# Optimization experiments

Measured on AMD Instinct MI355X. Metric: run time of the kernel, lower is better.

Reference implementation:

```python
import jax, jax.numpy as jnp
import numpy as np

N = 100000   # num variables
D_IN = 512
D_OUT = 512
C = 4096     # num clusters
K = 32       # vars per cluster
E = 16384    # cluster edges
S = 16       # shared vars per edge
H = 4        # num heads
NEG_SLOPE = 0.2


def setup_inputs() -> dict:
    key = jax.random.key(0)
    ks = jax.random.split(key, 8)
    xav = (6.0 / (D_IN + D_OUT)) ** 0.5  # xavier_uniform bound
    x_var = jax.random.normal(ks[0], (N, D_IN), dtype=jnp.float32)
    W_Q = jax.random.uniform(ks[1], (D_OUT, D_IN), jnp.float32, -xav, xav)
    W_K = jax.random.uniform(ks[2], (D_OUT, D_IN), jnp.float32, -xav, xav)
    W_V = jax.random.uniform(ks[3], (D_OUT, D_IN), jnp.float32, -xav, xav)
    head_weights = jnp.ones((H,), jnp.float32)
    cluster_var_ids = jax.random.randint(ks[4], (C, K), 0, N)
    cluster_edge_index = jax.random.randint(ks[5], (2, E), 0, C)
    shared_vars = jax.random.randint(ks[6], (E, S), 0, N)
    return {
        'x_var': x_var, 'W_Q': W_Q, 'W_K': W_K, 'W_V': W_V,
        'head_weights': head_weights,
        'cluster_var_ids': cluster_var_ids,
        'cluster_edge_index': cluster_edge_index,
        'shared_vars': shared_vars,
        'active_heads': 4,
    }


def reference(x_var, W_Q, W_K, W_V, head_weights,
              cluster_var_ids, cluster_edge_index, shared_vars, active_heads):
    # Per-cluster mean pooling over member variables: [C, D_in]
    cluster_feats = x_var[cluster_var_ids].mean(axis=1)
    # Linear projections (torch Linear: y = x @ W.T)
    Q = cluster_feats @ W_Q.T   # [C, D_out]
    Kc = cluster_feats @ W_K.T  # [C, D_out]
    V = cluster_feats @ W_V.T   # [C, D_out]
    c1 = cluster_edge_index[0]  # [E] source clusters
    c2 = cluster_edge_index[1]  # [E] target clusters
    # Scalar dot-product attention per cluster edge
    scale = jnp.asarray(D_OUT, jnp.float32) ** 0.5
    scores = jnp.einsum('ed,ed->e', Q[c1], Kc[c2]) / scale
    scores = jnp.where(scores >= 0, scores, NEG_SLOPE * scores)  # leaky_relu
    attn = jax.nn.sigmoid(scores) * head_weights[:active_heads].mean()  # [E]
    # Per-edge message = attn * V[c2], broadcast to each shared var of the edge
    upd = attn[:, None] * V[c2]                                   # [E, D_out]
    upd_flat = jnp.broadcast_to(upd[:, None, :], (E, S, D_OUT)).reshape(E * S, D_OUT)
    x_out = x_var.at[shared_vars.reshape(-1)].add(upd_flat)
    return x_out
```

## Files before the change

kernel.cpp:

```cpp
#include <hip/hip_runtime.h>
#include <hip/hip_bf16.h>
#include <math.h>

#define N_VARS    100000
#define D_DIM     512
#define C_CLUST   4096
#define K_VARS    32
#define E_EDGES   16384
#define S_SHARED  16
#define H_HEADS   4
#define CAP       32
#define NEG_SLOPE 0.2f

typedef __bf16 bf16x8_t __attribute__((ext_vector_type(8)));
typedef float  f32x4_t  __attribute__((ext_vector_type(4)));

__device__ __forceinline__ unsigned int f32_to_bf16_bits(float f) {
    unsigned int u = __builtin_bit_cast(unsigned int, f);
    unsigned int lsb = (u >> 16) & 1u;
    u += 0x7fffu + lsb;
    return u >> 16;
}
__device__ __forceinline__ unsigned int pack_bf16x2(float a, float b) {
    return (f32_to_bf16_bits(b) << 16) | f32_to_bf16_bits(a);
}
__device__ __forceinline__ float bf16_lo_to_f32(unsigned int w) {
    return __builtin_bit_cast(float, w << 16);
}
__device__ __forceinline__ float bf16_hi_to_f32(unsigned int w) {
    return __builtin_bit_cast(float, w & 0xffff0000u);
}

__device__ __forceinline__ int decode_active_heads(const int* p) {
    int raw = p[0];
    if (raw >= 1 && raw <= H_HEADS) return raw;
    float f = __builtin_bit_cast(float, raw);
    if (f >= 1.0f && f <= (float)H_HEADS) return (int)f;
    return H_HEADS;
}

__global__ void convert_w_kernel(const float* __restrict__ Wq,
                                 const float* __restrict__ Wk,
                                 const float* __restrict__ Wv,
                                 unsigned int* __restrict__ Wb) {
    const float* W = (blockIdx.y == 0) ? Wq : (blockIdx.y == 1) ? Wk : Wv;
    int i = blockIdx.x * blockDim.x + threadIdx.x;
    float2 w = ((const float2*)W)[i];
    Wb[(size_t)blockIdx.y * (D_DIM * D_DIM / 2) + i] = pack_bf16x2(w.x, w.y);
}

__global__ void pool_kernel(const float* __restrict__ x,
                            const int* __restrict__ cvid,
                            uint2* __restrict__ cfb ,
                            int* __restrict__ counts) {
    int gtid = blockIdx.x * blockDim.x + threadIdx.x;
    if (gtid < N_VARS) counts[gtid] = 0;

    int c = blockIdx.x * 2 + (threadIdx.x >> 7);
    c = __builtin_amdgcn_readfirstlane(c);
    int t = threadIdx.x & 127;
    const int* cv = cvid + c * K_VARS;
    float4 acc = {0.f, 0.f, 0.f, 0.f};
#pragma unroll 8
    for (int k = 0; k < K_VARS; ++k) {
        int v = cv[k];
        float4 w = ((const float4*)(x + (size_t)v * D_DIM))[t];
        acc.x += w.x; acc.y += w.y; acc.z += w.z; acc.w += w.w;
    }
    const float inv = 1.0f / (float)K_VARS;
    uint2 o;
    o.x = pack_bf16x2(acc.x * inv, acc.y * inv);
    o.y = pack_bf16x2(acc.z * inv, acc.w * inv);
    cfb[(size_t)c * (D_DIM / 4) + t] = o;
}

__global__ __launch_bounds__(256) void gemm_kernel(
        const unsigned short* __restrict__ cfb,
        const unsigned short* __restrict__ Wb,
        float* __restrict__ Qo, float* __restrict__ Ko,
        unsigned short* __restrict__ Vb) {
    const unsigned short* W = Wb + (size_t)blockIdx.z * D_DIM * D_DIM;

    int wave = threadIdx.x >> 6;
    int lane = threadIdx.x & 63;
    int m0 = blockIdx.x * 64 + wave * 16;
    int n0 = blockIdx.y * 64;
    int mr = m0 + (lane & 15);
    int kb = (lane >> 4) * 8;

    f32x4_t acc0 = {0.f,0.f,0.f,0.f}, acc1 = {0.f,0.f,0.f,0.f};
    f32x4_t acc2 = {0.f,0.f,0.f,0.f}, acc3 = {0.f,0.f,0.f,0.f};
    const unsigned short* arow = cfb + (size_t)mr * D_DIM + kb;
    const unsigned short* b0r  = W + (size_t)(n0 +  0 + (lane & 15)) * D_DIM + kb;
    const unsigned short* b1r  = W + (size_t)(n0 + 16 + (lane & 15)) * D_DIM + kb;
    const unsigned short* b2r  = W + (size_t)(n0 + 32 + (lane & 15)) * D_DIM + kb;
    const unsigned short* b3r  = W + (size_t)(n0 + 48 + (lane & 15)) * D_DIM + kb;
#pragma unroll 4
    for (int k0 = 0; k0 < D_DIM; k0 += 32) {
        bf16x8_t a  = *(const bf16x8_t*)(arow + k0);
        bf16x8_t b0 = *(const bf16x8_t*)(b0r + k0);
        bf16x8_t b1 = *(const bf16x8_t*)(b1r + k0);
        bf16x8_t b2 = *(const bf16x8_t*)(b2r + k0);
        bf16x8_t b3 = *(const bf16x8_t*)(b3r + k0);
        acc0 = __builtin_amdgcn_mfma_f32_16x16x32_bf16(a, b0, acc0, 0, 0, 0);
        acc1 = __builtin_amdgcn_mfma_f32_16x16x32_bf16(a, b1, acc1, 0, 0, 0);
        acc2 = __builtin_amdgcn_mfma_f32_16x16x32_bf16(a, b2, acc2, 0, 0, 0);
        acc3 = __builtin_amdgcn_mfma_f32_16x16x32_bf16(a, b3, acc3, 0, 0, 0);
    }
    int rb = m0 + (lane >> 4) * 4;
    int cl = lane & 15;
    if (blockIdx.z < 2) {
        float* O = (blockIdx.z == 0) ? Qo : Ko;
#pragma unroll
        for (int r = 0; r < 4; ++r) {
            float* orow = O + (size_t)(rb + r) * D_DIM + n0 + cl;
            orow[ 0] = acc0[r];
            orow[16] = acc1[r];
            orow[32] = acc2[r];
            orow[48] = acc3[r];
        }
    } else {
#pragma unroll
        for (int r = 0; r < 4; ++r) {
            unsigned short* orow = Vb + (size_t)(rb + r) * D_DIM + n0 + cl;
            orow[ 0] = (unsigned short)f32_to_bf16_bits(acc0[r]);
            orow[16] = (unsigned short)f32_to_bf16_bits(acc1[r]);
            orow[32] = (unsigned short)f32_to_bf16_bits(acc2[r]);
            orow[48] = (unsigned short)f32_to_bf16_bits(acc3[r]);
        }
    }
}

__global__ __launch_bounds__(256) void score_fill_kernel(
        const float* __restrict__ Q,
        const float* __restrict__ Kc,
        const int* __restrict__ cei,
        const float* __restrict__ hw,
        const int* __restrict__ active_heads,
        const int* __restrict__ shared_vars,
        int* __restrict__ counts,
        unsigned int* __restrict__ bucket) {
    int e = __builtin_amdgcn_readfirstlane(blockIdx.x * 4 + (threadIdx.x >> 6));
    int lane = threadIdx.x & 63;
    int c1 = cei[e];
    int c2 = cei[E_EDGES + e];
    const float4* q = (const float4*)(Q  + (size_t)c1 * D_DIM);
    const float4* k = (const float4*)(Kc + (size_t)c2 * D_DIM);
    float4 qa = q[lane], qb = q[lane + 64];
    float4 ka = k[lane], kb = k[lane + 64];
    float s = qa.x*ka.x + qa.y*ka.y + qa.z*ka.z + qa.w*ka.w
            + qb.x*kb.x + qb.y*kb.y + qb.z*kb.z + qb.w*kb.w;
#pragma unroll
    for (int off = 32; off > 0; off >>= 1)
        s += __shfl_xor(s, off);
    int ah = decode_active_heads(active_heads);
    float m = 0.f;
    for (int h = 0; h < ah; ++h) m += hw[h];
    m /= (float)ah;
    float sc = s * (1.0f / sqrtf((float)D_DIM));
    sc = sc >= 0.f ? sc : NEG_SLOPE * sc;
    float attn = m / (1.f + __expf(-sc));
    unsigned int packed = (f32_to_bf16_bits(attn) << 16) | (unsigned int)c2;
    if (lane < S_SHARED) {
        int v = shared_vars[e * S_SHARED + lane];
        int pos = atomicAdd(&counts[v], 1);
        if (pos < CAP) bucket[(size_t)v * CAP + pos] = packed;
    }
}

__global__ __launch_bounds__(256) void gather_kernel(
        const float* __restrict__ x,
        const unsigned short* __restrict__ V,
        const int* __restrict__ counts,
        const unsigned int* __restrict__ bucket,
        float* __restrict__ out) {
    int v = __builtin_amdgcn_readfirstlane(blockIdx.x * 4 + (threadIdx.x >> 6));
    int lane = threadIdx.x & 63;
    const f32x4_t* xr = (const f32x4_t*)(x + (size_t)v * D_DIM);
    f32x4_t a0 = xr[2 * lane];
    f32x4_t a1 = xr[2 * lane + 1];
    int cnt = counts[v];
    if (cnt > CAP) cnt = CAP;
    const unsigned int* bk = bucket + (size_t)v * CAP;
    uint4 pw = *(const uint4*)bk;

    int k = 0;
    while (k < cnt) {
        int m = cnt - k;
        uint4 w0, w1, w2, w3;
        w0 = ((const uint4*)(V + (size_t)(pw.x & 0xFFFu) * D_DIM))[lane];
        if (m > 1) w1 = ((const uint4*)(V + (size_t)(pw.y & 0xFFFu) * D_DIM))[lane];
        if (m > 2) w2 = ((const uint4*)(V + (size_t)(pw.z & 0xFFFu) * D_DIM))[lane];
        if (m > 3) w3 = ((const uint4*)(V + (size_t)(pw.w & 0xFFFu) * D_DIM))[lane];
        uint4 pwn;
        int kn = k + 4;
        if (kn < cnt) pwn = *(const uint4*)(bk + kn);

        float t0 = bf16_hi_to_f32(pw.x >> 16 << 16);
        {
            float at = __builtin_bit_cast(float, pw.x & 0xffff0000u);
            a0[0] += at * bf16_lo_to_f32(w0.x); a0[1] += at * bf16_hi_to_f32(w0.x);
            a0[2] += at * bf16_lo_to_f32(w0.y); a0[3] += at * bf16_hi_to_f32(w0.y);
            a1[0] += at * bf16_lo_to_f32(w0.z); a1[1] += at * bf16_hi_to_f32(w0.z);
            a1[2] += at * bf16_lo_to_f32(w0.w); a1[3] += at * bf16_hi_to_f32(w0.w);
        }
        if (m > 1) {
            float at = __builtin_bit_cast(float, pw.y & 0xffff0000u);
            a0[0] += at * bf16_lo_to_f32(w1.x); a0[1] += at * bf16_hi_to_f32(w1.x);
            a0[2] += at * bf16_lo_to_f32(w1.y); a0[3] += at * bf16_hi_to_f32(w1.y);
            a1[0] += at * bf16_lo_to_f32(w1.z); a1[1] += at * bf16_hi_to_f32(w1.z);
            a1[2] += at * bf16_lo_to_f32(w1.w); a1[3] += at * bf16_hi_to_f32(w1.w);
        }
        if (m > 2) {
            float at = __builtin_bit_cast(float, pw.z & 0xffff0000u);
            a0[0] += at * bf16_lo_to_f32(w2.x); a0[1] += at * bf16_hi_to_f32(w2.x);
            a0[2] += at * bf16_lo_to_f32(w2.y); a0[3] += at * bf16_hi_to_f32(w2.y);
            a1[0] += at * bf16_lo_to_f32(w2.z); a1[1] += at * bf16_hi_to_f32(w2.z);
            a1[2] += at * bf16_lo_to_f32(w2.w); a1[3] += at * bf16_hi_to_f32(w2.w);
        }
        if (m > 3) {
            float at = __builtin_bit_cast(float, pw.w & 0xffff0000u);
            a0[0] += at * bf16_lo_to_f32(w3.x); a0[1] += at * bf16_hi_to_f32(w3.x);
            a0[2] += at * bf16_lo_to_f32(w3.y); a0[3] += at * bf16_hi_to_f32(w3.y);
            a1[0] += at * bf16_lo_to_f32(w3.z); a1[1] += at * bf16_hi_to_f32(w3.z);
            a1[2] += at * bf16_lo_to_f32(w3.w); a1[3] += at * bf16_hi_to_f32(w3.w);
        }
        (void)t0;
        pw = pwn;
        k = kn;
    }
    f32x4_t* orow = (f32x4_t*)(out + (size_t)v * D_DIM);
    __builtin_nontemporal_store(a0, orow + 2 * lane);
    __builtin_nontemporal_store(a1, orow + 2 * lane + 1);
}

extern "C" void kernel_launch(void* const* d_in, const int* in_sizes, int n_in,
                              void* d_out, int out_size, void* d_ws, size_t ws_size,
                              hipStream_t stream) {
    const float* x_var = (const float*)d_in[0];
    const float* W_Q   = (const float*)d_in[1];
    const float* W_K   = (const float*)d_in[2];
    const float* W_V   = (const float*)d_in[3];
    const float* hw    = (const float*)d_in[4];
    const int* cvid  = (const int*)d_in[5];
    const int* cei   = (const int*)d_in[6];
    const int* shv   = (const int*)d_in[7];
    const int* ahp   = (const int*)d_in[8];

    char* ws = (char*)d_ws;
    const size_t MiB = 1024 * 1024;
    unsigned int* cfb = (unsigned int*)(ws + 0);
    unsigned int* Wb  = (unsigned int*)(ws + 4  * MiB);
    float* Q    = (float*)(ws + 6  * MiB);
    float* Kc   = (float*)(ws + 14 * MiB);
    unsigned short* Vb = (unsigned short*)(ws + 22 * MiB);
    int* counts = (int*)(ws + 30 * MiB + 65536);
    unsigned int* bucket = (unsigned int*)(ws + 31 * MiB);

    convert_w_kernel<<<dim3(D_DIM * D_DIM / 2 / 256, 3), 256, 0, stream>>>(
        W_Q, W_K, W_V, Wb);

    pool_kernel<<<C_CLUST / 2, 256, 0, stream>>>(x_var, cvid, (uint2*)cfb, counts);

    gemm_kernel<<<dim3(C_CLUST / 64, D_DIM / 64, 3), 256, 0, stream>>>(
        (const unsigned short*)cfb, (const unsigned short*)Wb, Q, Kc, Vb);

    score_fill_kernel<<<E_EDGES / 4, 256, 0, stream>>>(
        Q, Kc, cei, hw, ahp, shv, counts, bucket);

    gather_kernel<<<N_VARS / 4, 256, 0, stream>>>(x_var, Vb, counts, bucket,
                                                  (float*)d_out);
}
```

Measured before the change: 475.1 us.

## Reassociate QK scores via precomputed Wq^T Wk and bf16 intermediates

Replaces separate Q and K projections with a precomputed M = Wq^T Wk (small 512x512 GEMM on transposed bf16 weights) and a single T = cf·M^T projection, so scores become dot products of bf16 pooled features with bf16 T rows. This removes one large projection GEMM and halves score-kernel read traffic by storing intermediates in bf16 instead of fp32. It adds a transpose kernel and an extra GEMM launch, and introduces extra bf16 rounding of M. Gather also switches x loads to nontemporal.

New measurement: 483.6 us. Within noise of the previous version (+1.8%).

```diff
diff --git a/kernel.cpp b/kernel.cpp
--- a/kernel.cpp
+++ b/kernel.cpp
@@ -47,6 +47,25 @@
     int i = blockIdx.x * blockDim.x + threadIdx.x;
     float2 w = ((const float2*)W)[i];
     Wb[(size_t)blockIdx.y * (D_DIM * D_DIM / 2) + i] = pack_bf16x2(w.x, w.y);
+}
+
+__global__ void transpose_w_kernel(const float* __restrict__ Wq,
+                                   const float* __restrict__ Wk,
+                                   unsigned short* __restrict__ WqT,
+                                   unsigned short* __restrict__ WkT) {
+    __shared__ float tile[32][33];
+    const float* W = blockIdx.z ? Wk : Wq;
+    unsigned short* O = blockIdx.z ? WkT : WqT;
+    int r0 = blockIdx.y * 32, c0 = blockIdx.x * 32;
+    int tx = threadIdx.x & 31, ty = threadIdx.x >> 5;
+#pragma unroll
+    for (int i = 0; i < 32; i += 8)
+        tile[ty + i][tx] = W[(size_t)(r0 + ty + i) * D_DIM + c0 + tx];
+    __syncthreads();
+#pragma unroll
+    for (int i = 0; i < 32; i += 8)
+        O[(size_t)(c0 + ty + i) * D_DIM + r0 + tx] =
+            (unsigned short)f32_to_bf16_bits(tile[tx][ty + i]);
 }
 
 __global__ void pool_kernel(const float* __restrict__ x,
@@ -74,27 +93,24 @@
     cfb[(size_t)c * (D_DIM / 4) + t] = o;
 }
 
-__global__ __launch_bounds__(256) void gemm_kernel(
-        const unsigned short* __restrict__ cfb,
-        const unsigned short* __restrict__ Wb,
-        float* __restrict__ Qo, float* __restrict__ Ko,
-        unsigned short* __restrict__ Vb) {
-    const unsigned short* W = Wb + (size_t)blockIdx.z * D_DIM * D_DIM;
-
+__device__ __forceinline__ void gemm_tile_bf16out(
+        const unsigned short* __restrict__ A,
+        const unsigned short* __restrict__ B,
+        unsigned short* __restrict__ O,
+        int m0_block, int n0) {
     int wave = threadIdx.x >> 6;
     int lane = threadIdx.x & 63;
-    int m0 = blockIdx.x * 64 + wave * 16;
-    int n0 = blockIdx.y * 64;
+    int m0 = m0_block + wave * 16;
     int mr = m0 + (lane & 15);
     int kb = (lane >> 4) * 8;
 
     f32x4_t acc0 = {0.f,0.f,0.f,0.f}, acc1 = {0.f,0.f,0.f,0.f};
     f32x4_t acc2 = {0.f,0.f,0.f,0.f}, acc3 = {0.f,0.f,0.f,0.f};
-    const unsigned short* arow = cfb + (size_t)mr * D_DIM + kb;
-    const unsigned short* b0r  = W + (size_t)(n0 +  0 + (lane & 15)) * D_DIM + kb;
-    const unsigned short* b1r  = W + (size_t)(n0 + 16 + (lane & 15)) * D_DIM + kb;
-    const unsigned short* b2r  = W + (size_t)(n0 + 32 + (lane & 15)) * D_DIM + kb;
-    const unsigned short* b3r  = W + (size_t)(n0 + 48 + (lane & 15)) * D_DIM + kb;
+    const unsigned short* arow = A + (size_t)mr * D_DIM + kb;
+    const unsigned short* b0r  = B + (size_t)(n0 +  0 + (lane & 15)) * D_DIM + kb;
+    const unsigned short* b1r  = B + (size_t)(n0 + 16 + (lane & 15)) * D_DIM + kb;
+    const unsigned short* b2r  = B + (size_t)(n0 + 32 + (lane & 15)) * D_DIM + kb;
+    const unsigned short* b3r  = B + (size_t)(n0 + 48 + (lane & 15)) * D_DIM + kb;
 #pragma unroll 4
     for (int k0 = 0; k0 < D_DIM; k0 += 32) {
         bf16x8_t a  = *(const bf16x8_t*)(arow + k0);
@@ -109,31 +125,37 @@
     }
     int rb = m0 + (lane >> 4) * 4;
     int cl = lane & 15;
-    if (blockIdx.z < 2) {
-        float* O = (blockIdx.z == 0) ? Qo : Ko;
 #pragma unroll
-        for (int r = 0; r < 4; ++r) {
-            float* orow = O + (size_t)(rb + r) * D_DIM + n0 + cl;
-            orow[ 0] = acc0[r];
-            orow[16] = acc1[r];
-            orow[32] = acc2[r];
-            orow[48] = acc3[r];
-        }
-    } else {
-#pragma unroll
-        for (int r = 0; r < 4; ++r) {
-            unsigned short* orow = Vb + (size_t)(rb + r) * D_DIM + n0 + cl;
-            orow[ 0] = (unsigned short)f32_to_bf16_bits(acc0[r]);
-            orow[16] = (unsigned short)f32_to_bf16_bits(acc1[r]);
-            orow[32] = (unsigned short)f32_to_bf16_bits(acc2[r]);
-            orow[48] = (unsigned short)f32_to_bf16_bits(acc3[r]);
-        }
-    }
+    for (int r = 0; r < 4; ++r) {
+        unsigned short* orow = O + (size_t)(rb + r) * D_DIM + n0 + cl;
+        orow[ 0] = (unsigned short)f32_to_bf16_bits(acc0[r]);
+        orow[16] = (unsigned short)f32_to_bf16_bits(acc1[r]);
+        orow[32] = (unsigned short)f32_to_bf16_bits(acc2[r]);
+        orow[48] = (unsigned short)f32_to_bf16_bits(acc3[r]);
+    }
+}
+
+__global__ __launch_bounds__(256) void gemm_m_kernel(
+        const unsigned short* __restrict__ WqT,
+        const unsigned short* __restrict__ WkT,
+        unsigned short* __restrict__ Mb) {
+    gemm_tile_bf16out(WqT, WkT, Mb, blockIdx.x * 64, blockIdx.y * 64);
+}
+
+__global__ __launch_bounds__(256) void gemm_tv_kernel(
+        const unsigned short* __restrict__ cfb,
+        const unsigned short* __restrict__ Mb,
+        const unsigned short* __restrict__ Wvb,
+        unsigned short* __restrict__ Tb,
+        unsigned short* __restrict__ Vb) {
+    const unsigned short* B = (blockIdx.z == 0) ? Mb : Wvb;
+    unsigned short* O = (blockIdx.z == 0) ? Tb : Vb;
+    gemm_tile_bf16out(cfb, B, O, blockIdx.x * 64, blockIdx.y * 64);
 }
 
 __global__ __launch_bounds__(256) void score_fill_kernel(
-        const float* __restrict__ Q,
-        const float* __restrict__ Kc,
+        const unsigned short* __restrict__ cfb,
+        const unsigned short* __restrict__ Tb,
         const int* __restrict__ cei,
         const float* __restrict__ hw,
         const int* __restrict__ active_heads,
@@ -144,12 +166,16 @@
     int lane = threadIdx.x & 63;
     int c1 = cei[e];
     int c2 = cei[E_EDGES + e];
-    const float4* q = (const float4*)(Q  + (size_t)c1 * D_DIM);
-    const float4* k = (const float4*)(Kc + (size_t)c2 * D_DIM);
-    float4 qa = q[lane], qb = q[lane + 64];
-    float4 ka = k[lane], kb = k[lane + 64];
-    float s = qa.x*ka.x + qa.y*ka.y + qa.z*ka.z + qa.w*ka.w
-            + qb.x*kb.x + qb.y*kb.y + qb.z*kb.z + qb.w*kb.w;
+    uint4 qa = ((const uint4*)(cfb + (size_t)c1 * D_DIM))[lane];
+    uint4 ta = ((const uint4*)(Tb  + (size_t)c2 * D_DIM))[lane];
+    float s = bf16_lo_to_f32(qa.x) * bf16_lo_to_f32(ta.x)
+            + bf16_hi_to_f32(qa.x) * bf16_hi_to_f32(ta.x)
+            + bf16_lo_to_f32(qa.y) * bf16_lo_to_f32(ta.y)
+            + bf16_hi_to_f32(qa.y) * bf16_hi_to_f32(ta.y)
+            + bf16_lo_to_f32(qa.z) * bf16_lo_to_f32(ta.z)
+            + bf16_hi_to_f32(qa.z) * bf16_hi_to_f32(ta.z)
+            + bf16_lo_to_f32(qa.w) * bf16_lo_to_f32(ta.w)
+            + bf16_hi_to_f32(qa.w) * bf16_hi_to_f32(ta.w);
 #pragma unroll
     for (int off = 32; off > 0; off >>= 1)
         s += __shfl_xor(s, off);
@@ -177,8 +203,8 @@
     int v = __builtin_amdgcn_readfirstlane(blockIdx.x * 4 + (threadIdx.x >> 6));
     int lane = threadIdx.x & 63;
     const f32x4_t* xr = (const f32x4_t*)(x + (size_t)v * D_DIM);
-    f32x4_t a0 = xr[2 * lane];
-    f32x4_t a1 = xr[2 * lane + 1];
+    f32x4_t a0 = __builtin_nontemporal_load(xr + 2 * lane);
+    f32x4_t a1 = __builtin_nontemporal_load(xr + 2 * lane + 1);
     int cnt = counts[v];
     if (cnt > CAP) cnt = CAP;
     const unsigned int* bk = bucket + (size_t)v * CAP;
@@ -196,7 +222,6 @@
         int kn = k + 4;
         if (kn < cnt) pwn = *(const uint4*)(bk + kn);
 
-        float t0 = bf16_hi_to_f32(pw.x >> 16 << 16);
         {
             float at = __builtin_bit_cast(float, pw.x & 0xffff0000u);
             a0[0] += at * bf16_lo_to_f32(w0.x); a0[1] += at * bf16_hi_to_f32(w0.x);
@@ -225,7 +250,6 @@
             a1[0] += at * bf16_lo_to_f32(w3.z); a1[1] += at * bf16_hi_to_f32(w3.z);
             a1[2] += at * bf16_lo_to_f32(w3.w); a1[3] += at * bf16_hi_to_f32(w3.w);
         }
-        (void)t0;
         pw = pwn;
         k = kn;
     }
@@ -249,24 +273,32 @@
 
     char* ws = (char*)d_ws;
     const size_t MiB = 1024 * 1024;
-    unsigned int* cfb = (unsigned int*)(ws + 0);
-    unsigned int* Wb  = (unsigned int*)(ws + 4  * MiB);
-    float* Q    = (float*)(ws + 6  * MiB);
-    float* Kc   = (float*)(ws + 14 * MiB);
-    unsigned short* Vb = (unsigned short*)(ws + 22 * MiB);
-    int* counts = (int*)(ws + 30 * MiB + 65536);
-    unsigned int* bucket = (unsigned int*)(ws + 31 * MiB);
+    const size_t KiB = 1024;
+    unsigned int*   cfb  = (unsigned int*)(ws + 0);
+    unsigned int*   Wb   = (unsigned int*)(ws + 4 * MiB);
+    unsigned short* WqT  = (unsigned short*)(ws + 5 * MiB + 512*KiB);
+    unsigned short* WkT  = (unsigned short*)(ws + 6 * MiB);
+    unsigned short* Mb   = (unsigned short*)(ws + 7 * MiB);
+    unsigned short* Tb   = (unsigned short*)(ws + 8 * MiB);
+    unsigned short* Vb   = (unsigned short*)(ws + 12 * MiB);
+    int* counts          = (int*)(ws + 16 * MiB);
+    unsigned int* bucket = (unsigned int*)(ws + 17 * MiB);
 
     convert_w_kernel<<<dim3(D_DIM * D_DIM / 2 / 256, 3), 256, 0, stream>>>(
         W_Q, W_K, W_V, Wb);
 
+    transpose_w_kernel<<<dim3(16, 16, 2), 256, 0, stream>>>(W_Q, W_K, WqT, WkT);
+
     pool_kernel<<<C_CLUST / 2, 256, 0, stream>>>(x_var, cvid, (uint2*)cfb, counts);
 
-    gemm_kernel<<<dim3(C_CLUST / 64, D_DIM / 64, 3), 256, 0, stream>>>(
-        (const unsigned short*)cfb, (const unsigned short*)Wb, Q, Kc, Vb);
+    gemm_m_kernel<<<dim3(D_DIM / 64, D_DIM / 64), 256, 0, stream>>>(WqT, WkT, Mb);
+
+    gemm_tv_kernel<<<dim3(C_CLUST / 64, D_DIM / 64, 2), 256, 0, stream>>>(
+        (const unsigned short*)cfb, Mb,
+        (const unsigned short*)Wb + 2 * (size_t)D_DIM * D_DIM, Tb, Vb);
 
     score_fill_kernel<<<E_EDGES / 4, 256, 0, stream>>>(
-        Q, Kc, cei, hw, ahp, shv, counts, bucket);
+        (const unsigned short*)cfb, Tb, cei, hw, ahp, shv, counts, bucket);
 
     gather_kernel<<<N_VARS / 4, 256, 0, stream>>>(x_var, Vb, counts, bucket,
                                                   (float*)d_out);
```
